# Optimization experiments

Measured on AMD Instinct MI355X. Metric: run time of the kernel, lower is better.

Reference implementation:

```python
import jax, jax.numpy as jnp
import numpy as np

D_MODEL = 1024
N_HEADS = 16
HEAD_DIM = D_MODEL // N_HEADS


def setup_inputs() -> dict:
    key = jax.random.key(0)
    k_x, k_qkv, k_out = jax.random.split(key, 3)
    B, T = 4, 2048
    x = jax.random.normal(k_x, (B, T, D_MODEL), dtype=jnp.float32)
    # nn.Linear weight is (out, in); we store transposed (in, out) for x @ W
    s = 1.0 / np.sqrt(D_MODEL)
    W_qkv = jax.random.uniform(k_qkv, (D_MODEL, 3 * D_MODEL), dtype=jnp.float32, minval=-s, maxval=s)
    W_out = jax.random.uniform(k_out, (D_MODEL, D_MODEL), dtype=jnp.float32, minval=-s, maxval=s)
    return {"x": x, "W_qkv": W_qkv, "W_out": W_out}


def reference(x, W_qkv, W_out):
    B, T, C = x.shape
    H, Dh = N_HEADS, HEAD_DIM
    qkv = x @ W_qkv                                   # (B,T,3C)
    q, k, v = jnp.split(qkv, 3, axis=-1)
    # (B,T,C) -> (B,H,T,Dh)
    def split_heads(t):
        return t.reshape(B, T, H, Dh).transpose(0, 2, 1, 3)
    q, k, v = split_heads(q), split_heads(k), split_heads(v)
    scale = 1.0 / np.sqrt(Dh).astype(np.float32)
    scores = jnp.einsum('bhqd,bhkd->bhqk', q, k) * scale  # (B,H,T,T)
    causal = jnp.triu(jnp.ones((T, T), dtype=bool), k=1)   # True above diag
    scores = jnp.where(causal, -jnp.inf, scores)
    attn = jax.nn.softmax(scores, axis=-1)
    out = jnp.einsum('bhqk,bhkd->bhqd', attn, v)       # (B,H,T,Dh)
    out = out.transpose(0, 2, 1, 3).reshape(B, T, C)
    return out @ W_out
```

## Files before the change

kernel.cpp:

```cpp
#include <hip/hip_runtime.h>
#include <stdint.h>

#define T_ 2048
#define BB_ 4

typedef __bf16 bf16x8 __attribute__((ext_vector_type(8)));
typedef float f32x4 __attribute__((ext_vector_type(4)));
typedef unsigned short u16x8 __attribute__((ext_vector_type(8)));
typedef unsigned int u32x2 __attribute__((ext_vector_type(2)));
typedef unsigned int u32x4 __attribute__((ext_vector_type(4)));

__device__ __forceinline__ unsigned short f2b(float f) {
    unsigned int u = __builtin_bit_cast(unsigned int, f);
    return (unsigned short)((u + 0x7fffu + ((u >> 16) & 1u)) >> 16);
}

__device__ __forceinline__ unsigned cvt_pk(float lo, float hi) {
    unsigned r;
    asm("v_cvt_pk_bf16_f32 %0, %1, %2" : "=v"(r) : "v"(lo), "v"(hi));
    return r;
}

__device__ __forceinline__ void gload16(const void* g, const void* lds) {
    __builtin_amdgcn_global_load_lds(
        (__attribute__((address_space(1))) void*)(uintptr_t)g,
        (__attribute__((address_space(3))) void*)(uintptr_t)(unsigned int)(uintptr_t)lds,
        16, 0, 0);
}

__device__ __forceinline__ bf16x8 ld_b8(const unsigned short* p) {
    return *(const bf16x8*)p;
}

#define MFMA16(a, b, c) __builtin_amdgcn_mfma_f32_16x16x32_bf16((a), (b), (c), 0, 0, 0)

__global__ __launch_bounds__(256) void k_cvt(const float* __restrict__ in,
                                             unsigned short* __restrict__ out, int n) {
    int i = (blockIdx.x * 256 + threadIdx.x) * 4;
    const int stride = gridDim.x * 256 * 4;
    for (; i < n; i += stride) {
        const float4 v = *(const float4*)(in + i);
        ushort4 o = make_ushort4(f2b(v.x), f2b(v.y), f2b(v.z), f2b(v.w));
        *(ushort4*)(out + i) = o;
    }
}

template <int K, int N>
__global__ __launch_bounds__(256) void k_cvt_T(const float* __restrict__ W,
                                               unsigned short* __restrict__ WT) {
    __shared__ unsigned short t_[64][72];
    const int nt = blockIdx.x % (N / 64), kt = blockIdx.x / (N / 64);
    const int tid = threadIdx.x;
    const int r = tid >> 2, c = (tid & 3) * 16;
    const float* src = W + (size_t)(kt * 64 + r) * N + nt * 64 + c;
#pragma unroll
    for (int j = 0; j < 16; j += 4) {
        float4 v = *(const float4*)(src + j);
        t_[r][c + j + 0] = f2b(v.x);
        t_[r][c + j + 1] = f2b(v.y);
        t_[r][c + j + 2] = f2b(v.z);
        t_[r][c + j + 3] = f2b(v.w);
    }
    __syncthreads();
    unsigned short* dst = WT + (size_t)(nt * 64 + r) * K + kt * 64 + c;
#pragma unroll
    for (int j = 0; j < 16; ++j) dst[j] = t_[c + j][r];
}

template <int MODE, int NCOLS>
__global__ __launch_bounds__(512, 2) void k_gemm256(
    const unsigned short* __restrict__ A, const unsigned short* __restrict__ Bt,
    void* __restrict__ Cv, unsigned short* __restrict__ vt2) {
    constexpr int K = 1024, NT = K / 64;
    __shared__ unsigned short Abuf[3][2][8192];
    __shared__ unsigned short Bbuf[3][8192];
    const int tid = threadIdx.x;
    const int lane = tid & 63, wid = tid >> 6;
    const int wr = wid >> 1, wc = wid & 1;
    const int l4 = lane >> 4, l15 = lane & 15;
    const int m0 = blockIdx.y * 256, n0 = blockIdx.x * 128;

    const int se0 = tid * 8, se1 = tid * 8 + 4096;
    const int r0_ = se0 >> 6, c0_ = (se0 & 63) ^ ((r0_ & 7) << 3);
    const int r1_ = se1 >> 6, c1_ = (se1 & 63) ^ ((r1_ & 7) << 3);

    f32x4 acc[4][4] = {};

    auto STAGE1 = [&](int t, int d) {
        const unsigned short* as = A + (size_t)m0 * K + t * 64;
        gload16(as + (size_t)r0_ * K + c0_, &Abuf[d][0][se0]);
        gload16(as + (size_t)r1_ * K + c1_, &Abuf[d][0][se1]);
        const unsigned short* bs = Bt + (size_t)n0 * K + t * 64;
        gload16(bs + (size_t)r0_ * K + c0_, &Bbuf[d][se0]);
    };
    auto STAGE2 = [&](int t, int d) {
        const unsigned short* as = A + (size_t)(m0 + 128) * K + t * 64;
        gload16(as + (size_t)r0_ * K + c0_, &Abuf[d][1][se0]);
        gload16(as + (size_t)r1_ * K + c1_, &Abuf[d][1][se1]);
        const unsigned short* bs = Bt + (size_t)n0 * K + t * 64;
        gload16(bs + (size_t)r1_ * K + c1_, &Bbuf[d][se1]);
    };

    auto swz = [](const unsigned short* base, int row, int col) {
        int byte = row * 128 + col * 2;
        byte ^= (row & 7) << 4;
        return (const unsigned short*)((const char*)base + byte);
    };

    STAGE1(0, 0);
    STAGE2(0, 0);
    STAGE1(1, 1);
    STAGE2(1, 1);
    int d = 0;
    for (int t = 0; t < NT; ++t) {
        if (t == NT - 1)
            asm volatile("s_waitcnt vmcnt(0)" ::: "memory");
        else
            asm volatile("s_waitcnt vmcnt(6)" ::: "memory");
        __builtin_amdgcn_sched_barrier(0);
        __builtin_amdgcn_s_barrier();
        __builtin_amdgcn_sched_barrier(0);
        const int dn = (d + 2 >= 3) ? d - 1 : d + 2;
        if (t + 2 < NT) STAGE1(t + 2, dn);
        __builtin_amdgcn_sched_barrier(0);
        const unsigned short* Ah = &Abuf[d][wr >> 1][0];
        const unsigned short* Bh = &Bbuf[d][0];
        bf16x8 af[2][4], bfr[2][4];
#pragma unroll
        for (int ks = 0; ks < 2; ++ks) {
#pragma unroll
            for (int m = 0; m < 4; ++m)
                af[ks][m] =
                    ld_b8(swz(Ah, (wr & 1) * 64 + m * 16 + l15, ks * 32 + l4 * 8));
#pragma unroll
            for (int n = 0; n < 4; ++n)
                bfr[ks][n] = ld_b8(swz(Bh, wc * 64 + n * 16 + l15, ks * 32 + l4 * 8));
        }
        __builtin_amdgcn_s_setprio(1);
#pragma unroll
        for (int m = 0; m < 4; ++m)
#pragma unroll
            for (int n = 0; n < 4; ++n)
                acc[m][n] = MFMA16(af[0][m], bfr[0][n], acc[m][n]);
        __builtin_amdgcn_s_setprio(0);
        __builtin_amdgcn_sched_barrier(0);
        if (t + 2 < NT) STAGE2(t + 2, dn);
        __builtin_amdgcn_sched_barrier(0);
        __builtin_amdgcn_s_setprio(1);
#pragma unroll
        for (int m = 0; m < 4; ++m)
#pragma unroll
            for (int n = 0; n < 4; ++n)
                acc[m][n] = MFMA16(af[1][m], bfr[1][n], acc[m][n]);
        __builtin_amdgcn_s_setprio(0);
        d = (d + 1 == 3) ? 0 : d + 1;
    }

    const int crow0 = m0 + wr * 64 + l4 * 4;
    const int ccol0 = n0 + wc * 64 + l15;
    if (MODE == 0 && n0 >= 2048) {
#pragma unroll
        for (int m = 0; m < 4; ++m)
#pragma unroll
            for (int n = 0; n < 4; ++n) {
                const int row = crow0 + m * 16;
                const int c = ccol0 + n * 16 - 2048;
                const int b = row >> 11, tt = row & 2047;
                const int h = c >> 6, dh = c & 63;
                ushort4 o;
                o.x = f2b(acc[m][n][0]);
                o.y = f2b(acc[m][n][1]);
                o.z = f2b(acc[m][n][2]);
                o.w = f2b(acc[m][n][3]);
                *(ushort4*)(vt2 + (size_t)(b * 16 + h) * 131072 + (tt >> 2) * 256 +
                            dh * 4) = o;
            }
    } else {
#pragma unroll
        for (int m = 0; m < 4; ++m)
#pragma unroll
            for (int n = 0; n < 4; ++n)
#pragma unroll
                for (int r = 0; r < 4; ++r) {
                    const size_t idx =
                        (size_t)(crow0 + m * 16 + r) * NCOLS + ccol0 + n * 16;
                    if (MODE == 1)
                        ((float*)Cv)[idx] = acc[m][n][r];
                    else
                        ((unsigned short*)Cv)[idx] = f2b(acc[m][n][r]);
                }
    }
}

__global__ __launch_bounds__(256) void k_attn(const unsigned short* __restrict__ qkv,
                                              const unsigned short* __restrict__ vt2,
                                              unsigned short* __restrict__ ao) {
    __shared__ unsigned short Ks[2 * 4096];
    __shared__ unsigned short Vs[2 * 4096];
    const int bh = blockIdx.x & 63;
    const int p = blockIdx.x >> 6;
    const int b = bh >> 4, h = bh & 15;
    const int tid = threadIdx.x, lane = tid & 63, w = tid >> 6;
    const int l4 = lane >> 4, l15 = lane & 15;

    const int sr0 = w * 16 + (lane >> 3);
    const int scol = 8 * ((lane & 7) ^ (lane >> 3));
    const unsigned short* Kg = qkv + (size_t)(b * T_) * 3072 + 1024 + h * 64;

    const unsigned short* Vg = vt2 + (size_t)bh * 131072;
    const int s0v = (w * 2 + 0) * 2 + (lane >> 5);
    const int s1v = (w * 2 + 1) * 2 + (lane >> 5);
    const unsigned short* vsrc0 =
        Vg + (4 * (s0v & 3) + (s0v >> 2)) * 256 + (lane & 31) * 8;
    const unsigned short* vsrc1 =
        Vg + (4 * (s1v & 3) + (s1v >> 2)) * 256 + (lane & 31) * 8;

    const u32x4 onesw = {0x3f803f80u, 0x3f803f80u, 0x3f803f80u, 0x3f803f80u};
    const bf16x8 ones = __builtin_bit_cast(bf16x8, onesw);

    for (int half = 0; half < 2; ++half) {
        const int qt = half ? p : 31 - p;

        const unsigned short* qb =
            qkv + (size_t)(b * T_ + qt * 64 + w * 16 + l15) * 3072 + h * 64;
        bf16x8 qf0, qf1;
        {
            const bf16x8 r0 = ld_b8(qb + l4 * 8);
            const bf16x8 r1 = ld_b8(qb + 32 + l4 * 8);
#pragma unroll
            for (int j = 0; j < 8; ++j) {
                qf0[j] = (__bf16)((float)r0[j] * 0.18033688f);
                qf1[j] = (__bf16)((float)r1[j] * 0.18033688f);
            }
        }

        f32x4 o[4] = {};
        f32x4 o_l = {};

        auto STAGE = [&](int kt, int bi) {
            unsigned short* Kb = Ks + bi * 4096;
            unsigned short* Vb = Vs + bi * 4096;
            gload16(Kg + (size_t)(kt * 64 + sr0) * 3072 + scol, Kb + (w * 2) * 512);
            gload16(Kg + (size_t)(kt * 64 + sr0 + 8) * 3072 + scol, Kb + (w * 2 + 1) * 512);
            gload16(vsrc0 + kt * 4096, Vb + (w * 2) * 512);
            gload16(vsrc1 + kt * 4096, Vb + (w * 2 + 1) * 512);
        };

        auto COMPUTE = [&](int bi, bool masked) {
            const unsigned short* Kb = Ks + bi * 4096;
            const unsigned short* Vb = Vs + bi * 4096;
            float tv[4][4];
            __builtin_amdgcn_s_setprio(1);
#pragma unroll
            for (int i = 0; i < 4; ++i) {
                const int key = i * 16 + l15;
                const int sw = (key & 7) << 4;
                const bf16x8 kf0 = ld_b8(Kb + (key * 128 + ((l4 * 16) ^ sw)) / 2);
                const bf16x8 kf1 = ld_b8(Kb + (key * 128 + ((l4 * 16 + 64) ^ sw)) / 2);
                f32x4 sacc = {};
                sacc = MFMA16(kf0, qf0, sacc);
                sacc = MFMA16(kf1, qf1, sacc);
#pragma unroll
                for (int r = 0; r < 4; ++r) tv[i][r] = sacc[r];
            }
            __builtin_amdgcn_s_setprio(0);
            if (masked) {
#pragma unroll
                for (int i = 0; i < 4; ++i)
#pragma unroll
                    for (int r = 0; r < 4; ++r)
                        if (i * 16 + l4 * 4 + r > w * 16 + l15) tv[i][r] = -1e30f;
            }
            unsigned pw[8];
#pragma unroll
            for (int i = 0; i < 4; ++i) {
                float pv[4];
#pragma unroll
                for (int r = 0; r < 4; ++r) pv[r] = __builtin_amdgcn_exp2f(tv[i][r]);
                pw[i * 2 + 0] = cvt_pk(pv[0], pv[1]);
                pw[i * 2 + 1] = cvt_pk(pv[2], pv[3]);
            }
            __builtin_amdgcn_s_setprio(1);
#pragma unroll
            for (int st = 0; st < 2; ++st) {
                const u32x4 pk = {pw[st * 4 + 0], pw[st * 4 + 1], pw[st * 4 + 2],
                                  pw[st * 4 + 3]};
                const bf16x8 pf = __builtin_bit_cast(bf16x8, pk);
                o_l = MFMA16(pf, ones, o_l);
#pragma unroll
                for (int ni = 0; ni < 4; ++ni) {
                    const unsigned short* vb =
                        Vb + (l4 * 4 + st * 2) * 256 + (ni * 16 + l15) * 4;
                    const u32x2 va = *(const u32x2*)vb;
                    const u32x2 vc = *(const u32x2*)(vb + 256);
                    const u32x4 vv = {va.x, va.y, vc.x, vc.y};
                    const bf16x8 vf = __builtin_bit_cast(bf16x8, vv);
                    o[ni] = MFMA16(pf, vf, o[ni]);
                }
            }
            __builtin_amdgcn_s_setprio(0);
        };

        __syncthreads();
        STAGE(0, 0);
        __syncthreads();
        for (int kt = 0; kt < qt; ++kt) {
            STAGE(kt + 1, (kt + 1) & 1);
            COMPUTE(kt & 1, false);
            __syncthreads();
        }
        COMPUTE(qt & 1, true);

        unsigned short* aop = ao + (size_t)(b * T_ + qt * 64 + w * 16) * 1024 + h * 64;
#pragma unroll
        for (int r = 0; r < 4; ++r) {
            const float inv = 1.0f / o_l[r];
#pragma unroll
            for (int ni = 0; ni < 4; ++ni)
                aop[(size_t)(l4 * 4 + r) * 1024 + ni * 16 + l15] = f2b(o[ni][r] * inv);
        }
    }
}

extern "C" void kernel_launch(void* const* d_in, const int* in_sizes, int n_in,
                              void* d_out, int out_size, void* d_ws, size_t ws_size,
                              hipStream_t stream) {
    (void)in_sizes; (void)n_in; (void)out_size; (void)ws_size;
    const float* x = (const float*)d_in[0];
    const float* Wqkv = (const float*)d_in[1];
    const float* Wout = (const float*)d_in[2];
    char* ws = (char*)d_ws;
    unsigned short* xb = (unsigned short*)(ws + 0);
    unsigned short* wqkvT = (unsigned short*)(ws + 16777216);
    unsigned short* woutT = (unsigned short*)(ws + 23068672);
    unsigned short* qkvb = (unsigned short*)(ws + 25165824);
    unsigned short* vt2 = (unsigned short*)(ws + 75497472);
    unsigned short* ao = (unsigned short*)(ws + 92274688);

    k_cvt<<<2048, 256, 0, stream>>>(x, xb, 4 * T_ * 1024);
    k_cvt_T<1024, 3072><<<16 * 48, 256, 0, stream>>>(Wqkv, wqkvT);
    k_cvt_T<1024, 1024><<<16 * 16, 256, 0, stream>>>(Wout, woutT);
    k_gemm256<0, 3072><<<dim3(24, 32), 512, 0, stream>>>(xb, wqkvT, qkvb, vt2);
    k_attn<<<1024, 256, 0, stream>>>(qkvb, vt2, ao);
    k_gemm256<1, 1024><<<dim3(8, 32), 512, 0, stream>>>(ao, woutT, d_out, nullptr);
}
```

Baseline: 153.5 us.

## Use 128-query attention tiles with 8 waves and XCD-aware GEMM block remap

Doubles the attention query tile to 128 rows per block (8 waves of 512 threads), so each staged 64-key K/V tile in LDS serves twice as many queries and K/V global traffic halves. The causal mask now takes a per-wave diagonal offset, and the last two key tiles are masked. Separately, the GEMM remaps block IDs so consecutive blocks land on the same XCD chiplet, which should improve L2 reuse. The attention change halves the grid to 512 blocks and raises diagonal masking waste, which may reduce occupancy or load balance.

```diff
diff --git a/kernel.cpp b/kernel.cpp
--- a/kernel.cpp
+++ b/kernel.cpp
@@ -78,7 +78,10 @@
     const int lane = tid & 63, wid = tid >> 6;
     const int wr = wid >> 1, wc = wid & 1;
     const int l4 = lane >> 4, l15 = lane & 15;
-    const int m0 = blockIdx.y * 256, n0 = blockIdx.x * 128;
+    const int bid = blockIdx.y * gridDim.x + blockIdx.x;
+    const int cpx = (gridDim.x * gridDim.y) >> 3;
+    const int nb = (bid & 7) * cpx + (bid >> 3);
+    const int m0 = (nb / gridDim.x) * 256, n0 = (nb % gridDim.x) * 128;
 
     const int se0 = tid * 8, se1 = tid * 8 + 4096;
     const int r0_ = se0 >> 6, c0_ = (se0 & 63) ^ ((r0_ & 7) << 3);
@@ -192,7 +195,7 @@
     }
 }
 
-__global__ __launch_bounds__(256) void k_attn(const unsigned short* __restrict__ qkv,
+__global__ __launch_bounds__(512) void k_attn(const unsigned short* __restrict__ qkv,
                                               const unsigned short* __restrict__ vt2,
                                               unsigned short* __restrict__ ao) {
     __shared__ unsigned short Ks[2 * 4096];
@@ -202,27 +205,25 @@
     const int b = bh >> 4, h = bh & 15;
     const int tid = threadIdx.x, lane = tid & 63, w = tid >> 6;
     const int l4 = lane >> 4, l15 = lane & 15;
-
-    const int sr0 = w * 16 + (lane >> 3);
+    const int wrow = w * 16 + l15;
+
+    const int sr0 = w * 8 + (lane >> 3);
     const int scol = 8 * ((lane & 7) ^ (lane >> 3));
     const unsigned short* Kg = qkv + (size_t)(b * T_) * 3072 + 1024 + h * 64;
 
     const unsigned short* Vg = vt2 + (size_t)bh * 131072;
-    const int s0v = (w * 2 + 0) * 2 + (lane >> 5);
-    const int s1v = (w * 2 + 1) * 2 + (lane >> 5);
-    const unsigned short* vsrc0 =
-        Vg + (4 * (s0v & 3) + (s0v >> 2)) * 256 + (lane & 31) * 8;
-    const unsigned short* vsrc1 =
-        Vg + (4 * (s1v & 3) + (s1v >> 2)) * 256 + (lane & 31) * 8;
+    const int sv = w * 2 + (lane >> 5);
+    const unsigned short* vsrcw =
+        Vg + (4 * (sv & 3) + (sv >> 2)) * 256 + (lane & 31) * 8;
 
     const u32x4 onesw = {0x3f803f80u, 0x3f803f80u, 0x3f803f80u, 0x3f803f80u};
     const bf16x8 ones = __builtin_bit_cast(bf16x8, onesw);
 
     for (int half = 0; half < 2; ++half) {
-        const int qt = half ? p : 31 - p;
+        const int qq = half ? p : 15 - p;
 
         const unsigned short* qb =
-            qkv + (size_t)(b * T_ + qt * 64 + w * 16 + l15) * 3072 + h * 64;
+            qkv + (size_t)(b * T_ + qq * 128 + wrow) * 3072 + h * 64;
         bf16x8 qf0, qf1;
         {
             const bf16x8 r0 = ld_b8(qb + l4 * 8);
@@ -238,15 +239,12 @@
         f32x4 o_l = {};
 
         auto STAGE = [&](int kt, int bi) {
-            unsigned short* Kb = Ks + bi * 4096;
-            unsigned short* Vb = Vs + bi * 4096;
-            gload16(Kg + (size_t)(kt * 64 + sr0) * 3072 + scol, Kb + (w * 2) * 512);
-            gload16(Kg + (size_t)(kt * 64 + sr0 + 8) * 3072 + scol, Kb + (w * 2 + 1) * 512);
-            gload16(vsrc0 + kt * 4096, Vb + (w * 2) * 512);
-            gload16(vsrc1 + kt * 4096, Vb + (w * 2 + 1) * 512);
+            gload16(Kg + (size_t)(kt * 64 + sr0) * 3072 + scol,
+                    Ks + bi * 4096 + w * 512);
+            gload16(vsrcw + (size_t)kt * 4096, Vs + bi * 4096 + w * 512);
         };
 
-        auto COMPUTE = [&](int bi, bool masked) {
+        auto COMPUTE = [&](int bi, int dk) {
             const unsigned short* Kb = Ks + bi * 4096;
             const unsigned short* Vb = Vs + bi * 4096;
             float tv[4][4];
@@ -264,12 +262,13 @@
                 for (int r = 0; r < 4; ++r) tv[i][r] = sacc[r];
             }
             __builtin_amdgcn_s_setprio(0);
-            if (masked) {
+            if (dk >= 0) {
+                const int base = dk * 64 - wrow;
 #pragma unroll
                 for (int i = 0; i < 4; ++i)
 #pragma unroll
                     for (int r = 0; r < 4; ++r)
-                        if (i * 16 + l4 * 4 + r > w * 16 + l15) tv[i][r] = -1e30f;
+                        if (base + i * 16 + l4 * 4 + r > 0) tv[i][r] = -1e30f;
             }
             unsigned pw[8];
 #pragma unroll
@@ -301,17 +300,19 @@
             __builtin_amdgcn_s_setprio(0);
         };
 
+        const int NTI = 2 * qq + 1;
         __syncthreads();
         STAGE(0, 0);
         __syncthreads();
-        for (int kt = 0; kt < qt; ++kt) {
+        for (int kt = 0; kt < NTI; ++kt) {
             STAGE(kt + 1, (kt + 1) & 1);
-            COMPUTE(kt & 1, false);
+            COMPUTE(kt & 1, kt - 2 * qq);
             __syncthreads();
         }
-        COMPUTE(qt & 1, true);
-
-        unsigned short* aop = ao + (size_t)(b * T_ + qt * 64 + w * 16) * 1024 + h * 64;
+        COMPUTE(NTI & 1, 1);
+
+        unsigned short* aop =
+            ao + (size_t)(b * T_ + qq * 128 + w * 16) * 1024 + h * 64;
 #pragma unroll
         for (int r = 0; r < 4; ++r) {
             const float inv = 1.0f / o_l[r];
@@ -341,6 +342,6 @@
     k_cvt_T<1024, 3072><<<16 * 48, 256, 0, stream>>>(Wqkv, wqkvT);
     k_cvt_T<1024, 1024><<<16 * 16, 256, 0, stream>>>(Wout, woutT);
     k_gemm256<0, 3072><<<dim3(24, 32), 512, 0, stream>>>(xb, wqkvT, qkvb, vt2);
-    k_attn<<<1024, 256, 0, stream>>>(qkvb, vt2, ao);
+    k_attn<<<512, 512, 0, stream>>>(qkvb, vt2, ao);
     k_gemm256<1, 1024><<<dim3(8, 32), 512, 0, stream>>>(ao, woutT, d_out, nullptr);
 }
```

Result: faster. 144.7 us (-5.8%).
